# Performance work log

Measured on AMD Instinct MI355X. Metric: run time of the kernel, lower is better.

The kernel has to match this reference:

```python
import jax, jax.numpy as jnp
import numpy as np

B, L, D = 4, 2048, 768          # batch, seq_len, model dim
DI, DS, DTR, DCONV = 1536, 16, 48, 4  # d_inner, d_state, dt_rank, d_conv


def setup_inputs() -> dict:
    key = jax.random.key(0)
    ks = jax.random.split(key, 8)
    s = 0.02
    f32 = jnp.float32
    return {
        "x": jax.random.normal(ks[0], (B, L, D), f32),
        "ln_w": jnp.ones((D,), f32),
        "ln_b": jnp.zeros((D,), f32),
        "W_in": (jax.random.normal(ks[1], (D, 2 * DI), f32) * s),
        "conv_w": (jax.random.normal(ks[2], (DI, DCONV), f32) * s),
        "conv_b": jnp.zeros((DI,), f32),
        "W_x": (jax.random.normal(ks[3], (DI, DTR + 2 * DS), f32) * s),
        "W_dt": (jax.random.normal(ks[4], (DTR, DI), f32) * s),
        "b_dt": jnp.full((DI,), -4.6, f32),  # softplus(b_dt) ~ 0.01 init dt
        "A_log": jnp.log(jnp.tile(jnp.arange(1.0, DS + 1.0, dtype=f32), (DI, 1))),
        "D_param": jnp.ones((DI,), f32),
        "W_out": (jax.random.normal(ks[5], (DI, D), f32) * s),
    }


def reference(x, ln_w, ln_b, W_in, conv_w, conv_b, W_x, W_dt, b_dt,
              A_log, D_param, W_out):
    eps = 1e-5

    def layernorm(h):
        mu = h.mean(-1, keepdims=True)
        var = ((h - mu) ** 2).mean(-1, keepdims=True)
        return (h - mu) * jax.lax.rsqrt(var + eps) * ln_w + ln_b

    A = -jnp.exp(A_log)  # [DI, DS]

    def mixer(h):
        # h: [B, L, D]
        xz = h @ W_in                       # [B, L, 2*DI]
        u, z = jnp.split(xz, 2, axis=-1)    # each [B, L, DI]
        # causal depthwise conv1d (kernel DCONV)
        pad = jnp.pad(u, ((0, 0), (DCONV - 1, 0), (0, 0)))
        conv = conv_b
        for k in range(DCONV):
            conv = conv + pad[:, k:k + L, :] * conv_w[:, k]
        u = jax.nn.silu(conv)               # [B, L, DI]
        xdb = u @ W_x                       # [B, L, DTR+2*DS]
        dt_raw = xdb[..., :DTR]
        Bm = xdb[..., DTR:DTR + DS]         # [B, L, DS]
        Cm = xdb[..., DTR + DS:]            # [B, L, DS]
        dt = jax.nn.softplus(dt_raw @ W_dt + b_dt)  # [B, L, DI]

        def step(hst, inp):
            dt_t, B_t, C_t, u_t = inp       # [B,DI],[B,DS],[B,DS],[B,DI]
            dA = jnp.exp(dt_t[..., None] * A)              # [B,DI,DS]
            hst = hst * dA + (dt_t * u_t)[..., None] * B_t[:, None, :]
            y = jnp.einsum('bds,bs->bd', hst, C_t)
            return hst, y

        h0 = jnp.zeros((h.shape[0], DI, DS), u.dtype)
        xs = (jnp.swapaxes(dt, 0, 1), jnp.swapaxes(Bm, 0, 1),
              jnp.swapaxes(Cm, 0, 1), jnp.swapaxes(u, 0, 1))
        _, ys = jax.lax.scan(step, h0, xs)  # ys: [L, B, DI]
        y = jnp.swapaxes(ys, 0, 1) + u * D_param
        y = y * jax.nn.silu(z)
        return y @ W_out                    # [B, L, D]

    xn = layernorm(x)
    x_fwd = mixer(xn)
    x_bwd = jnp.flip(mixer(jnp.flip(xn, 1)), 1)
    return x + 0.5 * (x_fwd + x_bwd)
```

## Files before the change

### kernel.cpp

```cpp
#include <hip/hip_runtime.h>
#include <hip/hip_bf16.h>

#define B_  4
#define L_  2048
#define D_  768
#define DI_ 1536
#define DS_ 16
#define DTR_ 48
#define ROWS_ (B_*L_)

typedef __hip_bfloat16 bf16;
typedef __attribute__((ext_vector_type(8))) short bf16x8;
typedef __attribute__((ext_vector_type(4))) float f32x4;
typedef __attribute__((ext_vector_type(2))) float f32x2;

__device__ __forceinline__ float silu_f(float x) { return x / (1.f + __expf(-x)); }
__device__ __forceinline__ float softplus_f(float x) { return x > 15.f ? x : __logf(1.f + __expf(x)); }
__device__ __forceinline__ float b2f(bf16 v) { return __bfloat162float(v); }
__device__ __forceinline__ bf16 f2b(float v) { return __float2bfloat16(v); }
__device__ __forceinline__ float bfb(unsigned short u) {
    union { unsigned int i; float f; } w; w.i = ((unsigned int)u) << 16; return w.f;
}
__device__ __forceinline__ short f2bbits(float v) {
    bf16 t = __float2bfloat16(v);
    return *(short*)&t;
}
__device__ __forceinline__ void gload_lds16(const void* g, void* l) {
    __builtin_amdgcn_global_load_lds((const __attribute__((address_space(1))) void*)g,
                                     (__attribute__((address_space(3))) void*)l, 16, 0, 0);
}

__device__ __forceinline__ void pow_tree(float r, f32x2 pw[8]) {
    float r2 = r * r;
    f32x2 rr = {r2, r2};
    f32x2 r4 = rr * rr;
    f32x2 r8 = r4 * r4;
    pw[0] = (f32x2){r, r2};
    pw[1] = pw[0] * rr;
    pw[2] = pw[0] * r4;
    pw[3] = pw[1] * r4;
    pw[4] = pw[0] * r8;
    pw[5] = pw[1] * r8;
    pw[6] = pw[2] * r8;
    pw[7] = pw[3] * r8;
}

__global__ __launch_bounds__(256) void convert_wt(const float* __restrict__ W,
                                                  bf16* __restrict__ Wt,
                                                  int K, int N) {
    __shared__ float tile[32][33];
    int bx = blockIdx.x * 32;
    int by = blockIdx.y * 32;
    int tx = threadIdx.x & 31, ty = threadIdx.x >> 5;
#pragma unroll
    for (int i = 0; i < 32; i += 8)
        tile[ty + i][tx] = W[(size_t)(by + ty + i) * N + bx + tx];
    __syncthreads();
#pragma unroll
    for (int i = 0; i < 32; i += 8)
        Wt[(size_t)(bx + ty + i) * K + by + tx] = f2b(tile[tx][ty + i]);
}

__global__ __launch_bounds__(256) void convert_wxt(const float* __restrict__ W,
                                                   bf16* __restrict__ Wt) {
    int idx = blockIdx.x * 256 + threadIdx.x;
    int n = idx / DI_, k = idx % DI_;
    Wt[idx] = f2b(W[(size_t)k * 80 + n]);
}

__global__ __launch_bounds__(256) void convert_wdt(const float* __restrict__ W,
                                                   bf16* __restrict__ Wt) {
    int idx = blockIdx.x * 256 + threadIdx.x;
    int n = idx >> 6, k = idx & 63;
    Wt[idx] = f2b(k < DTR_ ? W[(size_t)k * DI_ + n] : 0.f);
}

__global__ __launch_bounds__(256) void ln_kernel(const float* __restrict__ x,
                                                 const float* __restrict__ w,
                                                 const float* __restrict__ b,
                                                 bf16* __restrict__ xn) {
    int row = blockIdx.x;
    const float* xr = x + (size_t)row * D_;
    bf16* on = xn + (size_t)row * D_;
    int t = threadIdx.x;
    float v[3];
    float s1 = 0.f, s2 = 0.f;
#pragma unroll
    for (int i = 0; i < 3; i++) { v[i] = xr[t + 256 * i]; s1 += v[i]; s2 += v[i] * v[i]; }
#pragma unroll
    for (int off = 32; off > 0; off >>= 1) { s1 += __shfl_down(s1, off); s2 += __shfl_down(s2, off); }
    __shared__ float sa[4], sb[4];
    int wid = t >> 6, lane = t & 63;
    if (lane == 0) { sa[wid] = s1; sb[wid] = s2; }
    __syncthreads();
    if (t == 0) { sa[0] = sa[0] + sa[1] + sa[2] + sa[3]; sb[0] = sb[0] + sb[1] + sb[2] + sb[3]; }
    __syncthreads();
    float mu = sa[0] * (1.f / D_);
    float var = sb[0] * (1.f / D_) - mu * mu;
    float rs = rsqrtf(var + 1e-5f);
#pragma unroll
    for (int i = 0; i < 3; i++) {
        int c = t + 256 * i;
        on[c] = f2b((v[i] - mu) * rs * w[c] + b[c]);
    }
}

__global__ __launch_bounds__(256) void gemm_in_mfma(const bf16* __restrict__ A,
                                                    const bf16* __restrict__ Bt,
                                                    bf16* __restrict__ u_pre,
                                                    bf16* __restrict__ z_s) {
    const int K = D_;
    constexpr int NX = (2 * DI_) / 128;
    constexpr int NWG = NX * (ROWS_ / 128);
    __shared__ __align__(16) short As[128 * 32];
    __shared__ __align__(16) short Bs[128 * 32];
    int tid = threadIdx.x;
    int lane = tid & 63, wid = tid >> 6;
    int wr = wid >> 1, wc = wid & 1;
    int bid = blockIdx.y * NX + blockIdx.x;
    bid = (bid & 7) * (NWG / 8) + (bid >> 3);
    int m0 = (bid / NX) * 128, n0 = (bid % NX) * 128;
    f32x4 acc[4][4];
#pragma unroll
    for (int i = 0; i < 4; i++)
#pragma unroll
        for (int j = 0; j < 4; j++) acc[i][j] = (f32x4){0.f, 0.f, 0.f, 0.f};

    int rl = lane & 15;
    int kb = (lane >> 4) * 8;

    for (int k0 = 0; k0 < K; k0 += 32) {
#pragma unroll
        for (int c = 0; c < 2; c++) {
            int s = c * 256 + tid;
            int r = s >> 2, sg = (s & 3) * 8;
            gload_lds16(A + (size_t)(m0 + r) * K + k0 + sg, &As[(c * 256 + wid * 64) * 8]);
            gload_lds16(Bt + (size_t)(n0 + r) * K + k0 + sg, &Bs[(c * 256 + wid * 64) * 8]);
        }
        __syncthreads();
        bf16x8 av[4], bv[4];
#pragma unroll
        for (int i = 0; i < 4; i++)
            av[i] = *(const bf16x8*)&As[(wr * 64 + i * 16 + rl) * 32 + kb];
#pragma unroll
        for (int j = 0; j < 4; j++)
            bv[j] = *(const bf16x8*)&Bs[(wc * 64 + j * 16 + rl) * 32 + kb];
#pragma unroll
        for (int i = 0; i < 4; i++)
#pragma unroll
            for (int j = 0; j < 4; j++)
                acc[i][j] = __builtin_amdgcn_mfma_f32_16x16x32_bf16(av[i], bv[j], acc[i][j], 0, 0, 0);
        __syncthreads();
    }
#pragma unroll
    for (int i = 0; i < 4; i++) {
        int mrow = m0 + wr * 64 + i * 16 + (lane >> 4) * 4;
#pragma unroll
        for (int j = 0; j < 4; j++) {
            int ncol = n0 + wc * 64 + j * 16 + rl;
#pragma unroll
            for (int r = 0; r < 4; r++) {
                float v = acc[i][j][r];
                int m = mrow + r;
                if (ncol < DI_) u_pre[(size_t)m * DI_ + ncol] = f2b(v);
                else            z_s[(size_t)m * DI_ + (ncol - DI_)] = f2b(silu_f(v));
            }
        }
    }
}

__global__ __launch_bounds__(256) void gemm_out_mfma(const bf16* __restrict__ gf,
                                                     const bf16* __restrict__ gb,
                                                     const bf16* __restrict__ Bt,
                                                     const float* __restrict__ resid,
                                                     float* __restrict__ C) {
    const int K = DI_, N = D_;
    constexpr int NX = D_ / 128;
    constexpr int NWG = NX * (ROWS_ / 128);
    __shared__ __align__(16) short As[128 * 32];
    __shared__ __align__(16) short Bs[128 * 32];
    int tid = threadIdx.x;
    int lane = tid & 63, wid = tid >> 6;
    int wr = wid >> 1, wc = wid & 1;
    int bid = blockIdx.y * NX + blockIdx.x;
    bid = (bid & 7) * (NWG / 8) + (bid >> 3);
    int m0 = (bid / NX) * 128, n0 = (bid % NX) * 128;
    f32x4 acc[4][4];
#pragma unroll
    for (int i = 0; i < 4; i++)
#pragma unroll
        for (int j = 0; j < 4; j++) acc[i][j] = (f32x4){0.f, 0.f, 0.f, 0.f};

    int rl = lane & 15;
    int kb = (lane >> 4) * 8;

    for (int k0 = 0; k0 < K; k0 += 32) {
#pragma unroll
        for (int c = 0; c < 2; c++) {
            int s = c * 256 + tid;
            int r = s >> 2, sg = (s & 3) * 8;
            size_t off = (size_t)(m0 + r) * K + k0 + sg;
            const unsigned short* pf = (const unsigned short*)(gf + off);
            const unsigned short* pb = (const unsigned short*)(gb + off);
            ushort4 a0 = *(const ushort4*)pf, a1 = *(const ushort4*)(pf + 4);
            ushort4 b0 = *(const ushort4*)pb, b1 = *(const ushort4*)(pb + 4);
            bf16x8 st;
            st[0] = f2bbits(bfb(a0.x) + bfb(b0.x));
            st[1] = f2bbits(bfb(a0.y) + bfb(b0.y));
            st[2] = f2bbits(bfb(a0.z) + bfb(b0.z));
            st[3] = f2bbits(bfb(a0.w) + bfb(b0.w));
            st[4] = f2bbits(bfb(a1.x) + bfb(b1.x));
            st[5] = f2bbits(bfb(a1.y) + bfb(b1.y));
            st[6] = f2bbits(bfb(a1.z) + bfb(b1.z));
            st[7] = f2bbits(bfb(a1.w) + bfb(b1.w));
            *(bf16x8*)&As[s * 8] = st;
            gload_lds16(Bt + (size_t)(n0 + r) * K + k0 + sg, &Bs[(c * 256 + wid * 64) * 8]);
        }
        __syncthreads();
        bf16x8 av[4], bv[4];
#pragma unroll
        for (int i = 0; i < 4; i++)
            av[i] = *(const bf16x8*)&As[(wr * 64 + i * 16 + rl) * 32 + kb];
#pragma unroll
        for (int j = 0; j < 4; j++)
            bv[j] = *(const bf16x8*)&Bs[(wc * 64 + j * 16 + rl) * 32 + kb];
#pragma unroll
        for (int i = 0; i < 4; i++)
#pragma unroll
            for (int j = 0; j < 4; j++)
                acc[i][j] = __builtin_amdgcn_mfma_f32_16x16x32_bf16(av[i], bv[j], acc[i][j], 0, 0, 0);
        __syncthreads();
    }
#pragma unroll
    for (int i = 0; i < 4; i++) {
        int mrow = m0 + wr * 64 + i * 16 + (lane >> 4) * 4;
#pragma unroll
        for (int j = 0; j < 4; j++) {
            int ncol = n0 + wc * 64 + j * 16 + rl;
#pragma unroll
            for (int r = 0; r < 4; r++) {
                size_t idx = (size_t)(mrow + r) * N + ncol;
                C[idx] = resid[idx] + 0.5f * acc[i][j][r];
            }
        }
    }
}

__global__ __launch_bounds__(256) void conv_kernel8(const bf16* __restrict__ up,
                                                    const float* __restrict__ cw,
                                                    const float* __restrict__ cb,
                                                    bf16* __restrict__ uf,
                                                    bf16* __restrict__ ub) {
    const int dpb = DI_ / 8;
    int idx = blockIdx.x * 256 + threadIdx.x;
    int d8 = (idx % dpb) * 8;
    int bl = idx / dpb;
    int l = bl % L_, b = bl / L_;
    const bf16* base = up + (size_t)b * L_ * DI_ + d8;
    float um[7][8];
#pragma unroll
    for (int k = 0; k < 7; k++) {
        int ll = l - 3 + k;
        if (ll >= 0 && ll < L_) {
            bf16x8 v = *(const bf16x8*)(base + (size_t)ll * DI_);
#pragma unroll
            for (int e = 0; e < 8; e++) um[k][e] = bfb((unsigned short)v[e]);
        } else {
#pragma unroll
            for (int e = 0; e < 8; e++) um[k][e] = 0.f;
        }
    }
    bf16x8 of, ob;
#pragma unroll
    for (int e = 0; e < 8; e++) {
        float4 w = *(const float4*)(cw + (size_t)(d8 + e) * 4);
        float bias = cb[d8 + e];
        float cf  = bias + um[0][e] * w.x + um[1][e] * w.y + um[2][e] * w.z + um[3][e] * w.w;
        float cbw = bias + um[6][e] * w.x + um[5][e] * w.y + um[4][e] * w.z + um[3][e] * w.w;
        of[e] = f2bbits(silu_f(cf));
        ob[e] = f2bbits(silu_f(cbw));
    }
    size_t oidx = (size_t)bl * DI_ + d8;
    *(bf16x8*)(uf + oidx) = of;
    *(bf16x8*)(ub + oidx) = ob;
}

__global__ __launch_bounds__(256) void xdb_mfma(const bf16* __restrict__ uf,
                                                const bf16* __restrict__ ub,
                                                const bf16* __restrict__ Wxt,
                                                float* __restrict__ xf,
                                                float* __restrict__ xb,
                                                bf16* __restrict__ drf,
                                                bf16* __restrict__ drb) {
    const bf16* u = blockIdx.y ? ub : uf;
    float* xout = blockIdx.y ? xb : xf;
    bf16* dout = blockIdx.y ? drb : drf;
    int m0 = blockIdx.x * 64;
    __shared__ __align__(16) short As[64 * 64];
    int tid = threadIdx.x;
    int lane = tid & 63, wid = tid >> 6;
    int rl = lane & 15, hi = lane >> 4;
    f32x4 acc[5];
#pragma unroll
    for (int j = 0; j < 5; j++) acc[j] = (f32x4){0.f, 0.f, 0.f, 0.f};

    int r_loc = wid * 16 + rl;

    for (int k0 = 0; k0 < DI_; k0 += 64) {
#pragma unroll
        for (int t = 0; t < 2; t++) {
            int s = t * 256 + tid;
            int row = s >> 3, c = s & 7;
            int cs = c ^ (row & 7);
            gload_lds16(u + (size_t)(m0 + row) * DI_ + k0 + cs * 8,
                        &As[(t * 256 + wid * 64) * 8]);
        }
        __syncthreads();
        bf16x8 av[2];
#pragma unroll
        for (int kc = 0; kc < 2; kc++) {
            int c = kc * 4 + hi;
            av[kc] = *(const bf16x8*)&As[r_loc * 64 + ((c ^ (r_loc & 7)) * 8)];
        }
#pragma unroll
        for (int j = 0; j < 5; j++)
#pragma unroll
            for (int kc = 0; kc < 2; kc++) {
                bf16x8 bv = *(const bf16x8*)(Wxt + (size_t)(j * 16 + rl) * DI_ + k0 + kc * 32 + hi * 8);
                acc[j] = __builtin_amdgcn_mfma_f32_16x16x32_bf16(av[kc], bv, acc[j], 0, 0, 0);
            }
        __syncthreads();
    }
#pragma unroll
    for (int j = 0; j < 5; j++) {
        int col = j * 16 + rl;
#pragma unroll
        for (int r = 0; r < 4; r++) {
            int m = m0 + wid * 16 + hi * 4 + r;
            float v = acc[j][r];
            if (col >= DTR_) xout[(size_t)m * 80 + col] = v;
            if (col < DTR_)      dout[(size_t)m * 64 + col] = f2b(v);
            else if (col < 64)   dout[(size_t)m * 64 + col] = f2b(0.f);
        }
    }
}

__global__ __launch_bounds__(256) void gemm_dt_mfma(const bf16* __restrict__ drf,
                                                    const bf16* __restrict__ drb,
                                                    const bf16* __restrict__ Wdt_t,
                                                    const float* __restrict__ bdt,
                                                    bf16* __restrict__ dtf,
                                                    bf16* __restrict__ dtb) {
    const bf16* A = blockIdx.z ? drb : drf;
    bf16* out = blockIdx.z ? dtb : dtf;
    int m0 = blockIdx.y * 64;
    int n0 = blockIdx.x * 256;
    __shared__ __align__(16) short As[64 * 64];
    int tid = threadIdx.x, lane = tid & 63, wid = tid >> 6;
    int rl = lane & 15, hi = lane >> 4;
#pragma unroll
    for (int t = 0; t < 2; t++) {
        int s = t * 256 + tid;
        int row = s >> 3, c = s & 7;
        gload_lds16(A + (size_t)(m0 + row) * 64 + (c ^ (row & 7)) * 8,
                    &As[(t * 256 + wid * 64) * 8]);
    }
    __syncthreads();
    int r_loc = wid * 16 + rl;
    bf16x8 av[2];
#pragma unroll
    for (int kc = 0; kc < 2; kc++) {
        int c = kc * 4 + hi;
        av[kc] = *(const bf16x8*)&As[r_loc * 64 + ((c ^ (r_loc & 7)) * 8)];
    }
    f32x4 acc[16];
#pragma unroll
    for (int j = 0; j < 16; j++) acc[j] = (f32x4){0.f, 0.f, 0.f, 0.f};
#pragma unroll
    for (int j = 0; j < 16; j++)
#pragma unroll
        for (int kc = 0; kc < 2; kc++) {
            bf16x8 bv = *(const bf16x8*)(Wdt_t + (size_t)(n0 + j * 16 + rl) * 64 + kc * 32 + hi * 8);
            acc[j] = __builtin_amdgcn_mfma_f32_16x16x32_bf16(av[kc], bv, acc[j], 0, 0, 0);
        }
#pragma unroll
    for (int j = 0; j < 16; j++) {
        int n = n0 + j * 16 + rl;
        float bb = bdt[n];
#pragma unroll
        for (int r = 0; r < 4; r++) {
            int m = m0 + wid * 16 + hi * 4 + r;
            out[(size_t)m * DI_ + n] = f2b(softplus_f(acc[j][r] + bb));
        }
    }
}

__global__ __launch_bounds__(256) void scan_part1(const bf16* __restrict__ dtf,
                                                  const bf16* __restrict__ dtb,
                                                  const bf16* __restrict__ uff,
                                                  const bf16* __restrict__ ubb,
                                                  const float* __restrict__ xdbf,
                                                  const float* __restrict__ xdbb,
                                                  const float* __restrict__ A_log,
                                                  float* __restrict__ Pbuf,
                                                  float* __restrict__ Ebuf,
                                                  int NC, int CL) {
    int dir = blockIdx.z;
    int b = blockIdx.y / NC, c = blockIdx.y % NC;
    int d = blockIdx.x * 256 + threadIdx.x;
    size_t cbase = (size_t)b * L_ * DI_ + d;
    const bf16* dt = (dir ? dtb : dtf) + cbase;
    const bf16* uu = (dir ? ubb : uff) + cbase;
    const float* xdb = (dir ? xdbb : xdbf) + (size_t)b * L_ * 80;

    float a[DS_];
    int fast = 1;
#pragma unroll
    for (int s = 0; s < DS_; s++) {
        a[s] = -__expf(A_log[d * DS_ + s]);
        fast = fast && (fabsf(a[s] + (float)(s + 1)) < 1e-4f * (s + 1));
    }
    fast = __syncthreads_and(fast);

    int t0 = c * CL;
    int l0 = dir ? (L_ - 1 - t0) : t0;
    int sD = dir ? -DI_ : DI_;
    int s80 = dir ? -80 : 80;
    const bf16* pdt = dt + (size_t)l0 * DI_;
    const bf16* pu  = uu + (size_t)l0 * DI_;
    const float* pbr = xdb + (size_t)l0 * 80 + DTR_;

    size_t base = (((size_t)(dir * B_ + b) * NC + c) * DS_) * DI_ + d;

    if (fast) {
        f32x2 h2[8];
#pragma unroll
        for (int k = 0; k < 8; k++) h2[k] = (f32x2){0.f, 0.f};
        float sdt = 0.f;
        for (int it = 0; it < CL; ++it) {
            float dtv = b2f(*pdt);
            float uv  = b2f(*pu);
            float xu = dtv * uv;
            sdt += dtv;
            float r = __expf(-dtv);
            f32x2 pw[8]; pow_tree(r, pw);
            float4 b0 = *(const float4*)(pbr);
            float4 b1 = *(const float4*)(pbr + 4);
            float4 b2v = *(const float4*)(pbr + 8);
            float4 b3 = *(const float4*)(pbr + 12);
            f32x2 B2[8] = {{b0.x, b0.y}, {b0.z, b0.w}, {b1.x, b1.y}, {b1.z, b1.w},
                           {b2v.x, b2v.y}, {b2v.z, b2v.w}, {b3.x, b3.y}, {b3.z, b3.w}};
            f32x2 xu2 = {xu, xu};
#pragma unroll
            for (int k = 0; k < 8; k++) h2[k] = h2[k] * pw[k] + xu2 * B2[k];
            pdt += sD; pu += sD; pbr += s80;
        }
        float Rc = __expf(-sdt);
        f32x2 pwP[8]; pow_tree(Rc, pwP);
#pragma unroll
        for (int k = 0; k < 8; k++) {
            Pbuf[base + (size_t)(2 * k) * DI_]     = pwP[k].x;
            Pbuf[base + (size_t)(2 * k + 1) * DI_] = pwP[k].y;
            Ebuf[base + (size_t)(2 * k) * DI_]     = h2[k].x;
            Ebuf[base + (size_t)(2 * k + 1) * DI_] = h2[k].y;
        }
    } else {
        float h[DS_], P[DS_];
#pragma unroll
        for (int s = 0; s < DS_; s++) { h[s] = 0.f; P[s] = 1.f; }
        for (int it = 0; it < CL; ++it) {
            float dtv = b2f(*pdt);
            float uv = b2f(*pu);
            float xu = dtv * uv;
            float4 b0 = *(const float4*)(pbr);
            float4 b1 = *(const float4*)(pbr + 4);
            float4 b2v = *(const float4*)(pbr + 8);
            float4 b3 = *(const float4*)(pbr + 12);
            float Bv[16] = {b0.x, b0.y, b0.z, b0.w, b1.x, b1.y, b1.z, b1.w,
                            b2v.x, b2v.y, b2v.z, b2v.w, b3.x, b3.y, b3.z, b3.w};
#pragma unroll
            for (int s = 0; s < DS_; s++) {
                float dA = __expf(dtv * a[s]);
                h[s] = h[s] * dA + xu * Bv[s];
                P[s] *= dA;
            }
            pdt += sD; pu += sD; pbr += s80;
        }
#pragma unroll
        for (int s = 0; s < DS_; s++) {
            Pbuf[base + (size_t)s * DI_] = P[s];
            Ebuf[base + (size_t)s * DI_] = h[s];
        }
    }
}

__global__ __launch_bounds__(256) void scan_part2(const float* __restrict__ Pbuf,
                                                  float* __restrict__ Ebuf,
                                                  int NC) {
    int idx = blockIdx.x * 256 + threadIdx.x;
    int d = idx % DI_;
    int rest = idx / DI_;
    int s = rest % DS_;
    int bb = rest / DS_;
    size_t base = ((size_t)bb * NC * DS_ + s) * DI_ + d;
    float H = 0.f;
    for (int c = 0; c < NC; c++) {
        size_t aa = base + (size_t)c * DS_ * DI_;
        float P = Pbuf[aa], E = Ebuf[aa];
        Ebuf[aa] = H;
        H = P * H + E;
    }
}

__global__ __launch_bounds__(256) void scan_part3(const bf16* __restrict__ dtf,
                                                  const bf16* __restrict__ dtb,
                                                  const bf16* __restrict__ uff,
                                                  const bf16* __restrict__ ubb,
                                                  const float* __restrict__ xdbf,
                                                  const float* __restrict__ xdbb,
                                                  const bf16* __restrict__ z_s,
                                                  const float* __restrict__ A_log,
                                                  const float* __restrict__ Dp_,
                                                  const float* __restrict__ Ebuf,
                                                  bf16* __restrict__ gf,
                                                  bf16* __restrict__ gb,
                                                  int NC, int CL) {
    int dir = blockIdx.z;
    int b = blockIdx.y / NC, c = blockIdx.y % NC;
    int d = blockIdx.x * 256 + threadIdx.x;
    size_t cbase = (size_t)b * L_ * DI_ + d;
    const bf16* dt = (dir ? dtb : dtf) + cbase;
    const bf16* uu = (dir ? ubb : uff) + cbase;
    const float* xdb = (dir ? xdbb : xdbf) + (size_t)b * L_ * 80;
    const bf16* zp = z_s + cbase;
    bf16* g = (dir ? gb : gf) + cbase;

    float a[DS_];
    int fast = 1;
#pragma unroll
    for (int s = 0; s < DS_; s++) {
        a[s] = -__expf(A_log[d * DS_ + s]);
        fast = fast && (fabsf(a[s] + (float)(s + 1)) < 1e-4f * (s + 1));
    }
    fast = __syncthreads_and(fast);
    float Dp = Dp_[d];

    size_t base = (((size_t)(dir * B_ + b) * NC + c) * DS_) * DI_ + d;

    int t0 = c * CL;
    int l0 = dir ? (L_ - 1 - t0) : t0;
    int sD = dir ? -DI_ : DI_;
    int s80 = dir ? -80 : 80;
    const bf16* pdt = dt + (size_t)l0 * DI_;
    const bf16* pu  = uu + (size_t)l0 * DI_;
    const bf16* pz  = zp + (size_t)l0 * DI_;
    bf16* pg = g + (size_t)l0 * DI_;
    const float* pbr = xdb + (size_t)l0 * 80 + DTR_;

    if (fast) {
        f32x2 h2[8];
#pragma unroll
        for (int k = 0; k < 8; k++)
            h2[k] = (f32x2){Ebuf[base + (size_t)(2 * k) * DI_],
                            Ebuf[base + (size_t)(2 * k + 1) * DI_]};
        for (int it = 0; it < CL; ++it) {
            float dtv = b2f(*pdt);
            float uv  = b2f(*pu);
            float zv  = b2f(*pz);
            float xu = dtv * uv;
            float r = __expf(-dtv);
            f32x2 pw[8]; pow_tree(r, pw);
            float4 b0 = *(const float4*)(pbr);
            float4 b1 = *(const float4*)(pbr + 4);
            float4 b2v = *(const float4*)(pbr + 8);
            float4 b3 = *(const float4*)(pbr + 12);
            float4 c0 = *(const float4*)(pbr + 16);
            float4 c1 = *(const float4*)(pbr + 20);
            float4 c2v = *(const float4*)(pbr + 24);
            float4 c3 = *(const float4*)(pbr + 28);
            f32x2 B2[8] = {{b0.x, b0.y}, {b0.z, b0.w}, {b1.x, b1.y}, {b1.z, b1.w},
                           {b2v.x, b2v.y}, {b2v.z, b2v.w}, {b3.x, b3.y}, {b3.z, b3.w}};
            f32x2 C2[8] = {{c0.x, c0.y}, {c0.z, c0.w}, {c1.x, c1.y}, {c1.z, c1.w},
                           {c2v.x, c2v.y}, {c2v.z, c2v.w}, {c3.x, c3.y}, {c3.z, c3.w}};
            f32x2 xu2 = {xu, xu};
            f32x2 y2 = {0.f, 0.f};
#pragma unroll
            for (int k = 0; k < 8; k++) {
                h2[k] = h2[k] * pw[k] + xu2 * B2[k];
                y2 = y2 + h2[k] * C2[k];
            }
            float y = y2.x + y2.y;
            *pg = f2b((y + uv * Dp) * zv);
            pdt += sD; pu += sD; pz += sD; pg += sD; pbr += s80;
        }
    } else {
        float h[DS_];
#pragma unroll
        for (int s = 0; s < DS_; s++) h[s] = Ebuf[base + (size_t)s * DI_];
        for (int it = 0; it < CL; ++it) {
            float dtv = b2f(*pdt);
            float uv = b2f(*pu);
            float zv = b2f(*pz);
            float xu = dtv * uv;
            float4 b0 = *(const float4*)(pbr);
            float4 b1 = *(const float4*)(pbr + 4);
            float4 b2v = *(const float4*)(pbr + 8);
            float4 b3 = *(const float4*)(pbr + 12);
            float4 c0 = *(const float4*)(pbr + 16);
            float4 c1 = *(const float4*)(pbr + 20);
            float4 c2v = *(const float4*)(pbr + 24);
            float4 c3 = *(const float4*)(pbr + 28);
            float Bv[16] = {b0.x, b0.y, b0.z, b0.w, b1.x, b1.y, b1.z, b1.w,
                            b2v.x, b2v.y, b2v.z, b2v.w, b3.x, b3.y, b3.z, b3.w};
            float Cv[16] = {c0.x, c0.y, c0.z, c0.w, c1.x, c1.y, c1.z, c1.w,
                            c2v.x, c2v.y, c2v.z, c2v.w, c3.x, c3.y, c3.z, c3.w};
            float y = 0.f;
#pragma unroll
            for (int s = 0; s < DS_; s++) {
                float dA = __expf(dtv * a[s]);
                h[s] = h[s] * dA + xu * Bv[s];
                y += h[s] * Cv[s];
            }
            *pg = f2b((y + uv * Dp) * zv);
            pdt += sD; pu += sD; pz += sD; pg += sD; pbr += s80;
        }
    }
}

__global__ __launch_bounds__(256) void scan_kernel(const bf16* __restrict__ dtf,
                                                   const bf16* __restrict__ dtb,
                                                   const bf16* __restrict__ uff,
                                                   const bf16* __restrict__ ubb,
                                                   const float* __restrict__ xdbf,
                                                   const float* __restrict__ xdbb,
                                                   const bf16* __restrict__ z_s,
                                                   const float* __restrict__ A_log,
                                                   const float* __restrict__ Dp_,
                                                   bf16* __restrict__ gf,
                                                   bf16* __restrict__ gb) {
    int dir = blockIdx.z;
    int b = blockIdx.y;
    int d = blockIdx.x * 256 + threadIdx.x;
    size_t cbase = (size_t)b * L_ * DI_ + d;
    const bf16* dt = (dir ? dtb : dtf) + cbase;
    const bf16* uu = (dir ? ubb : uff) + cbase;
    const float* xdb = (dir ? xdbb : xdbf) + (size_t)b * L_ * 80;
    const bf16* zp = z_s + cbase;
    bf16* g = (dir ? gb : gf) + cbase;
    float a[DS_];
#pragma unroll
    for (int s = 0; s < DS_; s++) a[s] = -__expf(A_log[d * DS_ + s]);
    float Dp = Dp_[d];
    float h[DS_];
#pragma unroll
    for (int s = 0; s < DS_; s++) h[s] = 0.f;
    for (int tt = 0; tt < L_; ++tt) {
        int l = dir ? (L_ - 1 - tt) : tt;
        size_t off = (size_t)l * DI_;
        float dtv = b2f(dt[off]);
        float uv = b2f(uu[off]);
        float zv = b2f(zp[off]);
        float xu = dtv * uv;
        const float* br = xdb + (size_t)l * 80 + DTR_;
        float y = 0.f;
#pragma unroll
        for (int s = 0; s < DS_; s++) {
            float dA = __expf(dtv * a[s]);
            h[s] = h[s] * dA + xu * br[s];
            y += h[s] * br[16 + s];
        }
        g[off] = f2b((y + uv * Dp) * zv);
    }
}

extern "C" void kernel_launch(void* const* d_in, const int* in_sizes, int n_in,
                              void* d_out, int out_size, void* d_ws, size_t ws_size,
                              hipStream_t stream) {
    const float* x      = (const float*)d_in[0];
    const float* ln_w   = (const float*)d_in[1];
    const float* ln_b   = (const float*)d_in[2];
    const float* W_in   = (const float*)d_in[3];
    const float* conv_w = (const float*)d_in[4];
    const float* conv_b = (const float*)d_in[5];
    const float* W_x    = (const float*)d_in[6];
    const float* W_dt   = (const float*)d_in[7];
    const float* b_dt   = (const float*)d_in[8];
    const float* A_log  = (const float*)d_in[9];
    const float* D_par  = (const float*)d_in[10];
    const float* W_out  = (const float*)d_in[11];
    float* out = (float*)d_out;

    const size_t NBbf = (size_t)ROWS_ * DI_ * sizeof(bf16);
    const size_t XDB4 = (size_t)ROWS_ * 80 * sizeof(float);
    const size_t WT1  = (size_t)D_ * 2 * DI_ * sizeof(bf16);
    const size_t WT2  = (size_t)DI_ * D_ * sizeof(bf16);
    const size_t WXT  = (size_t)80 * DI_ * sizeof(bf16);
    const size_t WDT  = (size_t)DI_ * 64 * sizeof(bf16);
    const size_t DR   = (size_t)ROWS_ * 64 * sizeof(bf16);
    const size_t BASE = 7 * NBbf + 2 * XDB4 + WT1 + WT2 + WXT + WDT + 2 * DR;
    if (ws_size < BASE) return;

    auto pe_bytes = [&](int NC) { return (size_t)2 * B_ * NC * DS_ * DI_ * sizeof(float); };
    int NC = 0;
    if (ws_size >= BASE + 2 * pe_bytes(32)) NC = 32;
    else if (ws_size >= BASE + 2 * pe_bytes(16)) NC = 16;
    const int CL = NC ? L_ / NC : 0;

    char* p = (char*)d_ws;
    bf16* z_s   = (bf16*)p;  p += NBbf;
    bf16* u_f   = (bf16*)p;  p += NBbf;
    bf16* u_b   = (bf16*)p;  p += NBbf;
    bf16* slotA = (bf16*)p;  p += NBbf;
    bf16* dt_b  = (bf16*)p;  p += NBbf;
    char* slotB = p;         p += NBbf;
    bf16* g_b   = (bf16*)p;  p += NBbf;
    float* xdb_f = (float*)p; p += XDB4;
    float* xdb_b = (float*)p; p += XDB4;
    bf16* Wt_in  = (bf16*)p;  p += WT1;
    bf16* Wt_out = (bf16*)p;  p += WT2;
    bf16* Wxt    = (bf16*)p;  p += WXT;
    bf16* Wdt_t  = (bf16*)p;  p += WDT;
    bf16* dr_f   = (bf16*)p;  p += DR;
    bf16* dr_b   = (bf16*)p;  p += DR;
    float* Pbuf = (float*)p;  p += NC ? pe_bytes(NC) : 0;
    float* Ebuf = (float*)p;

    bf16* u_pre = slotA;
    bf16* dt_f  = slotA;
    bf16* xn    = (bf16*)slotB;
    bf16* g_f   = (bf16*)slotB;

    convert_wt<<<dim3((2 * DI_) / 32, D_ / 32), 256, 0, stream>>>(W_in, Wt_in, D_, 2 * DI_);
    convert_wt<<<dim3(D_ / 32, DI_ / 32), 256, 0, stream>>>(W_out, Wt_out, DI_, D_);
    convert_wxt<<<(80 * DI_) / 256, 256, 0, stream>>>(W_x, Wxt);
    convert_wdt<<<(DI_ * 64) / 256, 256, 0, stream>>>(W_dt, Wdt_t);
    ln_kernel<<<ROWS_, 256, 0, stream>>>(x, ln_w, ln_b, xn);
    gemm_in_mfma<<<dim3((2 * DI_) / 128, ROWS_ / 128), 256, 0, stream>>>(xn, Wt_in, u_pre, z_s);
    conv_kernel8<<<(ROWS_ * DI_ / 8) / 256, 256, 0, stream>>>(u_pre, conv_w, conv_b, u_f, u_b);
    xdb_mfma<<<dim3(ROWS_ / 64, 2), 256, 0, stream>>>(u_f, u_b, Wxt, xdb_f, xdb_b, dr_f, dr_b);
    gemm_dt_mfma<<<dim3(DI_ / 256, ROWS_ / 64, 2), 256, 0, stream>>>(dr_f, dr_b, Wdt_t, b_dt, dt_f, dt_b);
    if (NC) {
        scan_part1<<<dim3(DI_ / 256, B_ * NC, 2), 256, 0, stream>>>(
            dt_f, dt_b, u_f, u_b, xdb_f, xdb_b, A_log, Pbuf, Ebuf, NC, CL);
        scan_part2<<<(2 * B_ * DS_ * DI_) / 256, 256, 0, stream>>>(Pbuf, Ebuf, NC);
        scan_part3<<<dim3(DI_ / 256, B_ * NC, 2), 256, 0, stream>>>(
            dt_f, dt_b, u_f, u_b, xdb_f, xdb_b, z_s, A_log, D_par, Ebuf, g_f, g_b, NC, CL);
    } else {
        scan_kernel<<<dim3(DI_ / 256, B_, 2), 256, 0, stream>>>(
            dt_f, dt_b, u_f, u_b, xdb_f, xdb_b, z_s, A_log, D_par, g_f, g_b);
    }
    gemm_out_mfma<<<dim3(D_ / 128, ROWS_ / 128), 256, 0, stream>>>(g_f, g_b, Wt_out, x, out);
}
```

Baseline: 385.4 us.

## Double-buffer LDS tiles in input, output and xdb GEMM kernels

```diff
diff --git a/kernel.cpp b/kernel.cpp
--- a/kernel.cpp
+++ b/kernel.cpp
@@ -110,10 +110,11 @@
                                                     bf16* __restrict__ u_pre,
                                                     bf16* __restrict__ z_s) {
     const int K = D_;
+    constexpr int KT = D_ / 32;
     constexpr int NX = (2 * DI_) / 128;
     constexpr int NWG = NX * (ROWS_ / 128);
-    __shared__ __align__(16) short As[128 * 32];
-    __shared__ __align__(16) short Bs[128 * 32];
+    __shared__ __align__(16) short As[2][128 * 32];
+    __shared__ __align__(16) short Bs[2][128 * 32];
     int tid = threadIdx.x;
     int lane = tid & 63, wid = tid >> 6;
     int wr = wid >> 1, wc = wid & 1;
@@ -128,23 +129,32 @@
 
     int rl = lane & 15;
     int kb = (lane >> 4) * 8;
-
-    for (int k0 = 0; k0 < K; k0 += 32) {
-#pragma unroll
-        for (int c = 0; c < 2; c++) {
-            int s = c * 256 + tid;
-            int r = s >> 2, sg = (s & 3) * 8;
-            gload_lds16(A + (size_t)(m0 + r) * K + k0 + sg, &As[(c * 256 + wid * 64) * 8]);
-            gload_lds16(Bt + (size_t)(n0 + r) * K + k0 + sg, &Bs[(c * 256 + wid * 64) * 8]);
-        }
-        __syncthreads();
+    int sr = tid >> 2, sg = (tid & 3) * 8;
+
+#pragma unroll
+    for (int c = 0; c < 2; c++) {
+        gload_lds16(A + (size_t)(m0 + c * 64 + sr) * K + 0 + sg, &As[0][(c * 256 + wid * 64) * 8]);
+        gload_lds16(Bt + (size_t)(n0 + c * 64 + sr) * K + 0 + sg, &Bs[0][(c * 256 + wid * 64) * 8]);
+    }
+    __syncthreads();
+
+    for (int kt = 0; kt < KT; kt++) {
+        int cur = kt & 1;
+        if (kt + 1 < KT) {
+            int k1 = (kt + 1) * 32;
+#pragma unroll
+            for (int c = 0; c < 2; c++) {
+                gload_lds16(A + (size_t)(m0 + c * 64 + sr) * K + k1 + sg, &As[cur ^ 1][(c * 256 + wid * 64) * 8]);
+                gload_lds16(Bt + (size_t)(n0 + c * 64 + sr) * K + k1 + sg, &Bs[cur ^ 1][(c * 256 + wid * 64) * 8]);
+            }
+        }
         bf16x8 av[4], bv[4];
 #pragma unroll
         for (int i = 0; i < 4; i++)
-            av[i] = *(const bf16x8*)&As[(wr * 64 + i * 16 + rl) * 32 + kb];
+            av[i] = *(const bf16x8*)&As[cur][(wr * 64 + i * 16 + rl) * 32 + kb];
 #pragma unroll
         for (int j = 0; j < 4; j++)
-            bv[j] = *(const bf16x8*)&Bs[(wc * 64 + j * 16 + rl) * 32 + kb];
+            bv[j] = *(const bf16x8*)&Bs[cur][(wc * 64 + j * 16 + rl) * 32 + kb];
 #pragma unroll
         for (int i = 0; i < 4; i++)
 #pragma unroll
@@ -175,10 +185,11 @@
                                                      const float* __restrict__ resid,
                                                      float* __restrict__ C) {
     const int K = DI_, N = D_;
+    constexpr int KT = DI_ / 32;
     constexpr int NX = D_ / 128;
     constexpr int NWG = NX * (ROWS_ / 128);
-    __shared__ __align__(16) short As[128 * 32];
-    __shared__ __align__(16) short Bs[128 * 32];
+    __shared__ __align__(16) short As[2][128 * 32];
+    __shared__ __align__(16) short Bs[2][128 * 32];
     int tid = threadIdx.x;
     int lane = tid & 63, wid = tid >> 6;
     int wr = wid >> 1, wc = wid & 1;
@@ -193,42 +204,67 @@
 
     int rl = lane & 15;
     int kb = (lane >> 4) * 8;
-
-    for (int k0 = 0; k0 < K; k0 += 32) {
+    int sr = tid >> 2, sg = (tid & 3) * 8;
+
+    auto conv_store = [&](int buf, ushort4 a0, ushort4 a1, ushort4 b0, ushort4 b1, int c) {
+        bf16x8 st;
+        st[0] = f2bbits(bfb(a0.x) + bfb(b0.x));
+        st[1] = f2bbits(bfb(a0.y) + bfb(b0.y));
+        st[2] = f2bbits(bfb(a0.z) + bfb(b0.z));
+        st[3] = f2bbits(bfb(a0.w) + bfb(b0.w));
+        st[4] = f2bbits(bfb(a1.x) + bfb(b1.x));
+        st[5] = f2bbits(bfb(a1.y) + bfb(b1.y));
+        st[6] = f2bbits(bfb(a1.z) + bfb(b1.z));
+        st[7] = f2bbits(bfb(a1.w) + bfb(b1.w));
+        *(bf16x8*)&As[buf][(c * 256 + tid) * 8] = st;
+    };
+
+    {
 #pragma unroll
         for (int c = 0; c < 2; c++) {
-            int s = c * 256 + tid;
-            int r = s >> 2, sg = (s & 3) * 8;
-            size_t off = (size_t)(m0 + r) * K + k0 + sg;
+            size_t off = (size_t)(m0 + c * 64 + sr) * K + 0 + sg;
             const unsigned short* pf = (const unsigned short*)(gf + off);
             const unsigned short* pb = (const unsigned short*)(gb + off);
             ushort4 a0 = *(const ushort4*)pf, a1 = *(const ushort4*)(pf + 4);
             ushort4 b0 = *(const ushort4*)pb, b1 = *(const ushort4*)(pb + 4);
-            bf16x8 st;
-            st[0] = f2bbits(bfb(a0.x) + bfb(b0.x));
-            st[1] = f2bbits(bfb(a0.y) + bfb(b0.y));
-            st[2] = f2bbits(bfb(a0.z) + bfb(b0.z));
-            st[3] = f2bbits(bfb(a0.w) + bfb(b0.w));
-            st[4] = f2bbits(bfb(a1.x) + bfb(b1.x));
-            st[5] = f2bbits(bfb(a1.y) + bfb(b1.y));
-            st[6] = f2bbits(bfb(a1.z) + bfb(b1.z));
-            st[7] = f2bbits(bfb(a1.w) + bfb(b1.w));
-            *(bf16x8*)&As[s * 8] = st;
-            gload_lds16(Bt + (size_t)(n0 + r) * K + k0 + sg, &Bs[(c * 256 + wid * 64) * 8]);
-        }
-        __syncthreads();
+            conv_store(0, a0, a1, b0, b1, c);
+            gload_lds16(Bt + (size_t)(n0 + c * 64 + sr) * K + 0 + sg, &Bs[0][(c * 256 + wid * 64) * 8]);
+        }
+    }
+    __syncthreads();
+
+    for (int kt = 0; kt < KT; kt++) {
+        int cur = kt & 1;
+        ushort4 ra0[2], ra1[2], rb0[2], rb1[2];
+        if (kt + 1 < KT) {
+            int k1 = (kt + 1) * 32;
+#pragma unroll
+            for (int c = 0; c < 2; c++) {
+                size_t off = (size_t)(m0 + c * 64 + sr) * K + k1 + sg;
+                const unsigned short* pf = (const unsigned short*)(gf + off);
+                const unsigned short* pb = (const unsigned short*)(gb + off);
+                ra0[c] = *(const ushort4*)pf; ra1[c] = *(const ushort4*)(pf + 4);
+                rb0[c] = *(const ushort4*)pb; rb1[c] = *(const ushort4*)(pb + 4);
+                gload_lds16(Bt + (size_t)(n0 + c * 64 + sr) * K + k1 + sg, &Bs[cur ^ 1][(c * 256 + wid * 64) * 8]);
+            }
+        }
         bf16x8 av[4], bv[4];
 #pragma unroll
         for (int i = 0; i < 4; i++)
-            av[i] = *(const bf16x8*)&As[(wr * 64 + i * 16 + rl) * 32 + kb];
+            av[i] = *(const bf16x8*)&As[cur][(wr * 64 + i * 16 + rl) * 32 + kb];
 #pragma unroll
         for (int j = 0; j < 4; j++)
-            bv[j] = *(const bf16x8*)&Bs[(wc * 64 + j * 16 + rl) * 32 + kb];
+            bv[j] = *(const bf16x8*)&Bs[cur][(wc * 64 + j * 16 + rl) * 32 + kb];
 #pragma unroll
         for (int i = 0; i < 4; i++)
 #pragma unroll
             for (int j = 0; j < 4; j++)
                 acc[i][j] = __builtin_amdgcn_mfma_f32_16x16x32_bf16(av[i], bv[j], acc[i][j], 0, 0, 0);
+        if (kt + 1 < KT) {
+#pragma unroll
+            for (int c = 0; c < 2; c++)
+                conv_store(cur ^ 1, ra0[c], ra1[c], rb0[c], rb1[c], c);
+        }
         __syncthreads();
     }
 #pragma unroll
@@ -296,7 +332,8 @@
     float* xout = blockIdx.y ? xb : xf;
     bf16* dout = blockIdx.y ? drb : drf;
     int m0 = blockIdx.x * 64;
-    __shared__ __align__(16) short As[64 * 64];
+    constexpr int KT = DI_ / 64;
+    __shared__ __align__(16) short As[2][64 * 64];
     int tid = threadIdx.x;
     int lane = tid & 63, wid = tid >> 6;
     int rl = lane & 15, hi = lane >> 4;
@@ -305,22 +342,34 @@
     for (int j = 0; j < 5; j++) acc[j] = (f32x4){0.f, 0.f, 0.f, 0.f};
 
     int r_loc = wid * 16 + rl;
-
-    for (int k0 = 0; k0 < DI_; k0 += 64) {
-#pragma unroll
-        for (int t = 0; t < 2; t++) {
-            int s = t * 256 + tid;
-            int row = s >> 3, c = s & 7;
-            int cs = c ^ (row & 7);
-            gload_lds16(u + (size_t)(m0 + row) * DI_ + k0 + cs * 8,
-                        &As[(t * 256 + wid * 64) * 8]);
-        }
-        __syncthreads();
+    int srow = tid >> 3, schunk = tid & 7;
+    int scs = schunk ^ (srow & 7);
+
+#pragma unroll
+    for (int t = 0; t < 2; t++)
+        gload_lds16(u + (size_t)(m0 + t * 32 + srow) * DI_ + 0 + ((schunk ^ ((t * 32 + srow) & 7)) * 8)
+                        - ((schunk ^ (srow & 7)) * 8) + scs * 8,
+                    &As[0][(t * 256 + wid * 64) * 8]);
+    __syncthreads();
+
+    for (int kt = 0; kt < KT; kt++) {
+        int cur = kt & 1;
+        if (kt + 1 < KT) {
+            int k1 = (kt + 1) * 64;
+#pragma unroll
+            for (int t = 0; t < 2; t++) {
+                int row = t * 32 + srow;
+                int cs = schunk ^ (row & 7);
+                gload_lds16(u + (size_t)(m0 + row) * DI_ + k1 + cs * 8,
+                            &As[cur ^ 1][(t * 256 + wid * 64) * 8]);
+            }
+        }
+        int k0 = kt * 64;
         bf16x8 av[2];
 #pragma unroll
         for (int kc = 0; kc < 2; kc++) {
             int c = kc * 4 + hi;
-            av[kc] = *(const bf16x8*)&As[r_loc * 64 + ((c ^ (r_loc & 7)) * 8)];
+            av[kc] = *(const bf16x8*)&As[cur][r_loc * 64 + ((c ^ (r_loc & 7)) * 8)];
         }
 #pragma unroll
         for (int j = 0; j < 5; j++)
```

Result: no change. 380.4 us (-1.3%).
